# Kernel tuning notes

Hardware: AMD Instinct MI355X
Metric: run time of the kernel (lower is better)

Reference implementation:

```python
import jax, jax.numpy as jnp
import numpy as np

D_MODEL = 1024
N_HEADS = 16
D_K = D_MODEL // N_HEADS
B, L = 2, 2048


def setup_inputs() -> dict:
    key = jax.random.key(0)
    ks = jax.random.split(key, 13)
    s = 0.02
    inp = {
        'query': jax.random.normal(ks[0], (B, L, D_MODEL), jnp.float32),
        'key': jax.random.normal(ks[1], (B, L, D_MODEL), jnp.float32),
        'value': jax.random.normal(ks[2], (B, L, D_MODEL), jnp.float32),
        'mask': jax.random.randint(ks[3], (1, 1, L, L), 0, 2).astype(bool),
        'W_q': jax.random.normal(ks[4], (D_MODEL, D_MODEL), jnp.float32) * s,
        'b_q': jnp.zeros((D_MODEL,), jnp.float32),
        'W_k': jax.random.normal(ks[5], (D_MODEL, D_MODEL), jnp.float32) * s,
        'b_k': jnp.zeros((D_MODEL,), jnp.float32),
        'W_v': jax.random.normal(ks[6], (D_MODEL, D_MODEL), jnp.float32) * s,
        'b_v': jnp.zeros((D_MODEL,), jnp.float32),
        'W_o': jax.random.normal(ks[7], (D_MODEL, D_MODEL), jnp.float32) * s,
        'b_o': jnp.zeros((D_MODEL,), jnp.float32),
    }
    return inp


def _split_heads(x):
    b, l, _ = x.shape
    return x.reshape(b, l, N_HEADS, D_K).transpose(0, 2, 1, 3)  # [B,H,L,dk]


def reference(query, key, value, mask, W_q, b_q, W_k, b_k, W_v, b_v, W_o, b_o):
    q = _split_heads(query @ W_q + b_q)
    k = _split_heads(key @ W_k + b_k)
    v = _split_heads(value @ W_v + b_v)
    # Unscaled attention logits [B,H,L,L] (NO 1/sqrt(dk))
    logits = jnp.einsum('bhqd,bhkd->bhqk', q, k)
    logits = jnp.where(mask, -jnp.inf, logits)
    w = jax.nn.softmax(logits, axis=-1)
    w = jnp.nan_to_num(w, nan=0.0)  # fully-masked rows -> zeros
    attended = jnp.einsum('bhqk,bhkd->bhqd', w, v)
    # dropout in eval mode = identity; combine heads
    out = attended.transpose(0, 2, 1, 3).reshape(B, L, D_MODEL)
    return out @ W_o + b_o
```

## Files before the change

kernel.cpp:

```cpp
#include <hip/hip_runtime.h>
#include <hip/hip_bf16.h>
#include <stdint.h>


typedef __bf16 bf16;
typedef __bf16 bf16x8 __attribute__((ext_vector_type(8)));
typedef float f32x4 __attribute__((ext_vector_type(4)));

#define AS1 __attribute__((address_space(1)))
#define AS3 __attribute__((address_space(3)))

__device__ __forceinline__ void g2l16(const void* g, void* l) {
    __builtin_amdgcn_global_load_lds((AS1 void*)g, (AS3 void*)l, 16, 0, 0);
}

__device__ __forceinline__ bool lane_masked(unsigned long long m) {
#if __has_builtin(__builtin_amdgcn_inverse_ballot_w64)
    return __builtin_amdgcn_inverse_ballot_w64(m);
#else
    return (m >> (threadIdx.x & 63)) & 1ull;
#endif
}

#define LOG2E 1.44269504088896f

__global__ __launch_bounds__(256) void cvt3_kernel(const float* __restrict__ a0,
                                                   const float* __restrict__ a1,
                                                   const float* __restrict__ a2,
                                                   bf16* o0, bf16* o1, bf16* o2) {
    int y = blockIdx.y;
    const float* in = (y == 0) ? a0 : (y == 1) ? a1 : a2;
    bf16* out = (y == 0) ? o0 : (y == 1) ? o1 : o2;
    int idx = blockIdx.x * 256 + threadIdx.x;
    float4 v = ((const float4*)in)[idx];
    __align__(8) bf16 o[4];
    o[0] = (bf16)v.x; o[1] = (bf16)v.y; o[2] = (bf16)v.z; o[3] = (bf16)v.w;
    *(uint2*)(out + (size_t)idx * 4) = *(const uint2*)o;
}

__global__ __launch_bounds__(256) void mdetect_kernel(const unsigned int* __restrict__ w,
                                                      int* __restrict__ flag) {
    int idx = blockIdx.x * 256 + threadIdx.x;
    unsigned v = w[idx];
    int f = 0;
    if (v == 0x3F800000u) f = 2;
    else if (v > 1u) f = 1;
    unsigned long long b1 = __ballot(f & 1);
    unsigned long long b2 = __ballot(f & 2);
    if ((threadIdx.x & 63) == 0) {
        int agg = (b1 ? 1 : 0) | (b2 ? 2 : 0);
        if (agg) atomicOr(flag, agg);
    }
}

__global__ __launch_bounds__(256) void mpack_kernel(const void* __restrict__ mask,
                                                    unsigned long long* __restrict__ mb,
                                                    const int* __restrict__ flag) {
    int idx = blockIdx.x * 256 + threadIdx.x;
    int f = *flag;
    bool v;
    if (f & 2)      v = ((const float*)mask)[idx] != 0.0f;
    else if (f & 1) v = ((const unsigned char*)mask)[idx] != 0;
    else            v = ((const int*)mask)[idx] != 0;
    unsigned long long b = __ballot(v);
    if ((threadIdx.x & 63) == 0) mb[idx >> 6] = b;
}

__global__ __launch_bounds__(256) void rpack_kernel(const unsigned long long* __restrict__ mb,
                                                    unsigned long long* __restrict__ rmb) {
    int task = blockIdx.x * 4 + (threadIdx.x >> 6);
    int qg = task >> 5, kt = task & 31;
    int lane = threadIdx.x & 63, quad = lane >> 4, col = lane & 15;
    #pragma unroll
    for (int r = 0; r < 4; ++r) {
        unsigned long long wrow = mb[(size_t)(qg * 16 + quad * 4 + r) * 32 + kt];
        #pragma unroll
        for (int nt = 0; nt < 4; ++nt) {
            unsigned long long b = __ballot(((wrow >> (nt * 16 + col)) & 1ull) != 0);
            if (lane == 0) rmb[(size_t)task * 16 + r * 4 + nt] = b;
        }
    }
}

__global__ __launch_bounds__(256) void wtrans_kernel(const float* W0, const float* W1,
                                                     const float* W2, const float* W3,
                                                     bf16* T0, bf16* T1, bf16* T2, bf16* T3) {
    const float* W; bf16* T;
    int y = blockIdx.y;
    if (y == 0)      { W = W0; T = T0; }
    else if (y == 1) { W = W1; T = T1; }
    else if (y == 2) { W = W2; T = T2; }
    else             { W = W3; T = T3; }
    int tx = blockIdx.x & 15, ty = blockIdx.x >> 4;
    int n0 = tx * 64, k0 = ty * 64;
    __shared__ __align__(16) bf16 t[64 * 72];
    int tid = threadIdx.x;
    #pragma unroll
    for (int rr = 0; rr < 4; ++rr) {
        int idx = rr * 256 + tid;
        int r = idx >> 4, c4 = (idx & 15) * 4;
        float4 v = *(const float4*)(W + (size_t)(k0 + r) * 1024 + n0 + c4);
        __align__(8) bf16 o[4];
        o[0] = (bf16)v.x; o[1] = (bf16)v.y; o[2] = (bf16)v.z; o[3] = (bf16)v.w;
        *(uint2*)&t[r * 72 + c4] = *(const uint2*)o;
    }
    __syncthreads();
    #pragma unroll
    for (int rr = 0; rr < 2; ++rr) {
        int idx = rr * 256 + tid;
        int n = idx >> 3, kc = (idx & 7) * 8;
        __align__(16) bf16 o[8];
        #pragma unroll
        for (int j = 0; j < 8; ++j) o[j] = t[(kc + j) * 72 + n];
        *(uint4*)(T + (size_t)(n0 + n) * 1024 + k0 + kc) = *(const uint4*)o;
    }
}

template <int MODE>
__device__ __forceinline__ void gemm128_core(const bf16* __restrict__ A,
                                             const bf16* __restrict__ Bt,
                                             const float* __restrict__ bias,
                                             void* __restrict__ Out, int bm, int bn,
                                             float scale) {
    __shared__ __align__(16) bf16 la[128 * 32];
    __shared__ __align__(16) bf16 lb[128 * 32];
    int tid = threadIdx.x;
    int w = tid >> 6, lane = tid & 63;
    int quad = lane >> 4, col = lane & 15;
    int wm = w >> 1, wn = w & 1;
    int m0 = bm * 128, n0 = bn * 128;
    f32x4 acc[4][4];
    f32x4 z = {0.f, 0.f, 0.f, 0.f};
    #pragma unroll
    for (int i = 0; i < 4; ++i)
        #pragma unroll
        for (int j = 0; j < 4; ++j) acc[i][j] = z;
    int srow = lane >> 2;
    int skc = (lane & 3) * 8;
    for (int kt = 0; kt < 32; ++kt) {
        int kk = kt * 32;
        __syncthreads();
        #pragma unroll
        for (int rr = 0; rr < 2; ++rr) {
            int ch = rr * 4 + w;
            int row = ch * 16 + srow;
            g2l16(A + (size_t)(m0 + row) * 1024 + kk + skc, &la[ch * 512]);
            g2l16(Bt + (size_t)(n0 + row) * 1024 + kk + skc, &lb[ch * 512]);
        }
        __syncthreads();
        bf16x8 af[4], bfr[4];
        #pragma unroll
        for (int mt = 0; mt < 4; ++mt)
            af[mt] = *(const bf16x8*)&la[(wm * 64 + mt * 16 + col) * 32 + quad * 8];
        #pragma unroll
        for (int nt = 0; nt < 4; ++nt)
            bfr[nt] = *(const bf16x8*)&lb[(wn * 64 + nt * 16 + col) * 32 + quad * 8];
        #pragma unroll
        for (int mt = 0; mt < 4; ++mt)
            #pragma unroll
            for (int nt = 0; nt < 4; ++nt)
                acc[mt][nt] = __builtin_amdgcn_mfma_f32_16x16x32_bf16(
                    af[mt], bfr[nt], acc[mt][nt], 0, 0, 0);
    }
    float bia[4];
    #pragma unroll
    for (int nt = 0; nt < 4; ++nt) bia[nt] = bias[n0 + wn * 64 + nt * 16 + col];
    #pragma unroll
    for (int mt = 0; mt < 4; ++mt) {
        #pragma unroll
        for (int nt = 0; nt < 4; ++nt) {
            #pragma unroll
            for (int r = 0; r < 4; ++r) {
                int m = m0 + wm * 64 + mt * 16 + quad * 4 + r;
                int n = n0 + wn * 64 + nt * 16 + col;
                float v = (acc[mt][nt][r] + bia[nt]) * scale;
                if (MODE == 0) {
                    int b = m >> 11, l = m & 2047, h = n >> 6, d = n & 63;
                    ((bf16*)Out)[(((size_t)b * 16 + h) * 2048 + l) * 64 + d] = (bf16)v;
                } else {
                    int b = m >> 11, l = m & 2047, h = n >> 6, d = n & 63;
                    ((bf16*)Out)[(((size_t)b * 16 + h) * 64 + d) * 2048 + l] = (bf16)v;
                }
            }
        }
    }
}

__global__ __launch_bounds__(256) void qkv_kernel(
    const bf16* Xq, const bf16* Xk, const bf16* Xv,
    const bf16* Wq, const bf16* Wk, const bf16* Wv,
    const float* bq, const float* bk, const float* bv,
    bf16* Qh, bf16* Kh, bf16* Vt) {
    int y = blockIdx.y;
    int bm = blockIdx.x >> 3, bn = blockIdx.x & 7;
    if (y == 0)      gemm128_core<0>(Xq, Wq, bq, Qh, bm, bn, LOG2E);
    else if (y == 1) gemm128_core<0>(Xk, Wk, bk, Kh, bm, bn, 1.0f);
    else             gemm128_core<2>(Xv, Wv, bv, Vt, bm, bn, 1.0f);
}

__global__ __launch_bounds__(256) void ogemm_kernel(const bf16* __restrict__ A,
                                                    const bf16* __restrict__ Wt,
                                                    const float* __restrict__ bias,
                                                    float* __restrict__ Out) {
    int bm = blockIdx.x >> 3, bn = blockIdx.x & 7;
    __shared__ __align__(16) bf16 la[64 * 32];
    __shared__ __align__(16) bf16 lb[128 * 32];
    int tid = threadIdx.x;
    int w = tid >> 6, lane = tid & 63;
    int quad = lane >> 4, col = lane & 15;
    int m0 = bm * 64, n0 = bn * 128;
    f32x4 acc[4][2];
    f32x4 z = {0.f, 0.f, 0.f, 0.f};
    #pragma unroll
    for (int i = 0; i < 4; ++i) { acc[i][0] = z; acc[i][1] = z; }
    int srow = lane >> 2;
    int skc = (lane & 3) * 8;
    for (int kt = 0; kt < 32; ++kt) {
        int kk = kt * 32;
        __syncthreads();
        g2l16(A + (size_t)(m0 + w * 16 + srow) * 1024 + kk + skc, &la[w * 512]);
        #pragma unroll
        for (int rr = 0; rr < 2; ++rr) {
            int ch = rr * 4 + w;
            g2l16(Wt + (size_t)(n0 + ch * 16 + srow) * 1024 + kk + skc, &lb[ch * 512]);
        }
        __syncthreads();
        bf16x8 af[4], bfr[2];
        #pragma unroll
        for (int mt = 0; mt < 4; ++mt)
            af[mt] = *(const bf16x8*)&la[(mt * 16 + col) * 32 + quad * 8];
        #pragma unroll
        for (int nt = 0; nt < 2; ++nt)
            bfr[nt] = *(const bf16x8*)&lb[(w * 32 + nt * 16 + col) * 32 + quad * 8];
        #pragma unroll
        for (int mt = 0; mt < 4; ++mt)
            #pragma unroll
            for (int nt = 0; nt < 2; ++nt)
                acc[mt][nt] = __builtin_amdgcn_mfma_f32_16x16x32_bf16(
                    af[mt], bfr[nt], acc[mt][nt], 0, 0, 0);
    }
    float bia[2];
    bia[0] = bias[n0 + w * 32 + col];
    bia[1] = bias[n0 + w * 32 + 16 + col];
    #pragma unroll
    for (int mt = 0; mt < 4; ++mt)
        #pragma unroll
        for (int nt = 0; nt < 2; ++nt)
            #pragma unroll
            for (int r = 0; r < 4; ++r)
                Out[(size_t)(m0 + mt * 16 + quad * 4 + r) * 1024 +
                    n0 + w * 32 + nt * 16 + col] = acc[mt][nt][r] + bia[nt];
}

__global__ __launch_bounds__(128) void attn_kernel(const bf16* __restrict__ Qh,
                                                   const bf16* __restrict__ Kh,
                                                   const bf16* __restrict__ Vt,
                                                   const unsigned long long* __restrict__ rmb,
                                                   bf16* __restrict__ att) {
    int bh = blockIdx.x, qt = blockIdx.y;
    int b = bh >> 4, h = bh & 15;
    int q0 = qt * 64;
    __shared__ __align__(16) bf16 ks[64 * 64];
    __shared__ __align__(16) bf16 vs[64 * 64];
    __shared__ __align__(16) bf16 ps[2 * 32 * 72];
    int tid = threadIdx.x;
    int w = tid >> 6, lane = tid & 63;
    int quad = lane >> 4, col = lane & 15;
    int c7 = col & 7;
    int sr = lane >> 3;
    int sg = (lane & 7) ^ sr;
    int swz0 = (quad ^ c7) * 8;
    int swz1 = ((4 + quad) ^ c7) * 8;

    int mofs = __builtin_amdgcn_readfirstlane((qt * 4 + w * 2) * 512);

    #pragma unroll
    for (int i = 0; i < 4; ++i) {
        int ch = w * 4 + i;
        g2l16(Qh + ((size_t)bh * 2048 + q0 + ch * 8 + sr) * 64 + sg * 8, &ks[ch * 512]);
    }
    __syncthreads();
    bf16x8 aq[2][2];
    #pragma unroll
    for (int mt = 0; mt < 2; ++mt) {
        aq[mt][0] = *(const bf16x8*)&ks[(w * 32 + mt * 16 + col) * 64 + swz0];
        aq[mt][1] = *(const bf16x8*)&ks[(w * 32 + mt * 16 + col) * 64 + swz1];
    }
    bf16x8 onesf;
    #pragma unroll
    for (int i = 0; i < 8; ++i) onesf[i] = (bf16)1.0f;

    f32x4 z = {0.f, 0.f, 0.f, 0.f};
    f32x4 O[2][4], R[2];
    #pragma unroll
    for (int mt = 0; mt < 2; ++mt) {
        R[mt] = z;
        #pragma unroll
        for (int i = 0; i < 4; ++i) O[mt][i] = z;
    }

    for (int kt = 0; kt < 32; ++kt) {
        __syncthreads();
        #pragma unroll
        for (int i = 0; i < 4; ++i) {
            int ch = w * 4 + i;
            int r = ch * 8 + sr;
            g2l16(Kh + ((size_t)bh * 2048 + kt * 64 + r) * 64 + sg * 8, &ks[ch * 512]);
            g2l16(Vt + ((size_t)bh * 64 + r) * 2048 + kt * 64 + sg * 8, &vs[ch * 512]);
        }
        __syncthreads();

        f32x4 s[2][4];
        #pragma unroll
        for (int nt = 0; nt < 4; ++nt) {
            s[0][nt] = z; s[1][nt] = z;
            bf16x8 bk0 = *(const bf16x8*)&ks[(nt * 16 + col) * 64 + swz0];
            s[0][nt] = __builtin_amdgcn_mfma_f32_16x16x32_bf16(aq[0][0], bk0, s[0][nt], 0, 0, 0);
            s[1][nt] = __builtin_amdgcn_mfma_f32_16x16x32_bf16(aq[1][0], bk0, s[1][nt], 0, 0, 0);
            bf16x8 bk1 = *(const bf16x8*)&ks[(nt * 16 + col) * 64 + swz1];
            s[0][nt] = __builtin_amdgcn_mfma_f32_16x16x32_bf16(aq[0][1], bk1, s[0][nt], 0, 0, 0);
            s[1][nt] = __builtin_amdgcn_mfma_f32_16x16x32_bf16(aq[1][1], bk1, s[1][nt], 0, 0, 0);
        }

        #pragma unroll
        for (int mt = 0; mt < 2; ++mt) {
            const unsigned long long* mw = rmb + mofs + mt * 512 + kt * 16;
            #pragma unroll
            for (int r = 0; r < 4; ++r) {
                #pragma unroll
                for (int nt = 0; nt < 4; ++nt) {
                    float p = __builtin_amdgcn_exp2f(s[mt][nt][r]);
                    if (lane_masked(mw[r * 4 + nt])) p = 0.0f;
                    ps[w * 2304 + (mt * 16 + quad * 4 + r) * 72 + nt * 16 + col] = (bf16)p;
                }
            }
        }

        bf16x8 ap[2][2];
        #pragma unroll
        for (int mt = 0; mt < 2; ++mt) {
            ap[mt][0] = *(const bf16x8*)&ps[w * 2304 + (mt * 16 + col) * 72 + quad * 8];
            ap[mt][1] = *(const bf16x8*)&ps[w * 2304 + (mt * 16 + col) * 72 + 32 + quad * 8];
        }
        #pragma unroll
        for (int dt = 0; dt < 4; ++dt) {
            bf16x8 bv0 = *(const bf16x8*)&vs[(dt * 16 + col) * 64 + swz0];
            O[0][dt] = __builtin_amdgcn_mfma_f32_16x16x32_bf16(ap[0][0], bv0, O[0][dt], 0, 0, 0);
            O[1][dt] = __builtin_amdgcn_mfma_f32_16x16x32_bf16(ap[1][0], bv0, O[1][dt], 0, 0, 0);
            bf16x8 bv1 = *(const bf16x8*)&vs[(dt * 16 + col) * 64 + swz1];
            O[0][dt] = __builtin_amdgcn_mfma_f32_16x16x32_bf16(ap[0][1], bv1, O[0][dt], 0, 0, 0);
            O[1][dt] = __builtin_amdgcn_mfma_f32_16x16x32_bf16(ap[1][1], bv1, O[1][dt], 0, 0, 0);
        }
        #pragma unroll
        for (int mt = 0; mt < 2; ++mt) {
            R[mt] = __builtin_amdgcn_mfma_f32_16x16x32_bf16(ap[mt][0], onesf, R[mt], 0, 0, 0);
            R[mt] = __builtin_amdgcn_mfma_f32_16x16x32_bf16(ap[mt][1], onesf, R[mt], 0, 0, 0);
        }
    }

    #pragma unroll
    for (int mt = 0; mt < 2; ++mt) {
        #pragma unroll
        for (int r = 0; r < 4; ++r) {
            float rsv = R[mt][r];
            float inv = (rsv > 0.f) ? 1.0f / rsv : 0.f;
            int qg = q0 + w * 32 + mt * 16 + quad * 4 + r;
            #pragma unroll
            for (int dt = 0; dt < 4; ++dt) {
                float ov = O[mt][dt][r] * inv;
                att[((size_t)b * 2048 + qg) * 1024 + h * 64 + dt * 16 + col] = (bf16)ov;
            }
        }
    }
}

extern "C" void kernel_launch(void* const* d_in, const int* in_sizes, int n_in,
                              void* d_out, int out_size, void* d_ws, size_t ws_size,
                              hipStream_t stream) {
    (void)in_sizes; (void)n_in; (void)out_size; (void)ws_size;
    const float* query = (const float*)d_in[0];
    const float* key_  = (const float*)d_in[1];
    const float* value = (const float*)d_in[2];
    const void*  mask  = d_in[3];
    const float* W_q = (const float*)d_in[4];
    const float* b_q = (const float*)d_in[5];
    const float* W_k = (const float*)d_in[6];
    const float* b_k = (const float*)d_in[7];
    const float* W_v = (const float*)d_in[8];
    const float* b_v = (const float*)d_in[9];
    const float* W_o = (const float*)d_in[10];
    const float* b_o = (const float*)d_in[11];

    char* ws = (char*)d_ws;
    bf16* Xq  = (bf16*)(ws + 0);
    bf16* Xk  = (bf16*)(ws + 8388608);
    bf16* Xv  = (bf16*)(ws + 16777216);
    bf16* Wtq = (bf16*)(ws + 25165824);
    bf16* Wtk = (bf16*)(ws + 27262976);
    bf16* Wtv = (bf16*)(ws + 29360128);
    bf16* Wto = (bf16*)(ws + 31457280);
    bf16* Qh  = (bf16*)(ws + 33554432);
    bf16* Kh  = (bf16*)(ws + 41943040);
    bf16* Vt  = (bf16*)(ws + 50331648);
    bf16* att = (bf16*)(ws + 58720256);
    unsigned long long* mb  = (unsigned long long*)(ws + 67108864);
    unsigned long long* rmb = (unsigned long long*)(ws + 67633152);
    int* flag = (int*)(ws + 68157440);

    hipMemsetAsync(flag, 0, 4, stream);
    mdetect_kernel<<<4096, 256, 0, stream>>>((const unsigned int*)mask, flag);
    mpack_kernel<<<16384, 256, 0, stream>>>(mask, mb, flag);
    rpack_kernel<<<1024, 256, 0, stream>>>(mb, rmb);

    cvt3_kernel<<<dim3(4096, 3), 256, 0, stream>>>(query, key_, value, Xq, Xk, Xv);
    wtrans_kernel<<<dim3(256, 4), 256, 0, stream>>>(W_q, W_k, W_v, W_o, Wtq, Wtk, Wtv, Wto);

    qkv_kernel<<<dim3(256, 3), 256, 0, stream>>>(Xq, Xk, Xv, Wtq, Wtk, Wtv,
                                                 b_q, b_k, b_v, Qh, Kh, Vt);
    attn_kernel<<<dim3(32, 32), 128, 0, stream>>>(Qh, Kh, Vt, rmb, att);
    ogemm_kernel<<<512, 256, 0, stream>>>(att, Wto, b_o, (float*)d_out);
}
```

Before: 271.8 us.

## Fuse input conversion into GEMMs, split attention over keys, merge mask packing

Measured after the change: 297.4 us. +9.4%, slower.

```diff
diff --git a/kernel.cpp b/kernel.cpp
--- a/kernel.cpp
+++ b/kernel.cpp
@@ -23,20 +23,6 @@
 }
 
 #define LOG2E 1.44269504088896f
-
-__global__ __launch_bounds__(256) void cvt3_kernel(const float* __restrict__ a0,
-                                                   const float* __restrict__ a1,
-                                                   const float* __restrict__ a2,
-                                                   bf16* o0, bf16* o1, bf16* o2) {
-    int y = blockIdx.y;
-    const float* in = (y == 0) ? a0 : (y == 1) ? a1 : a2;
-    bf16* out = (y == 0) ? o0 : (y == 1) ? o1 : o2;
-    int idx = blockIdx.x * 256 + threadIdx.x;
-    float4 v = ((const float4*)in)[idx];
-    __align__(8) bf16 o[4];
-    o[0] = (bf16)v.x; o[1] = (bf16)v.y; o[2] = (bf16)v.z; o[3] = (bf16)v.w;
-    *(uint2*)(out + (size_t)idx * 4) = *(const uint2*)o;
-}
 
 __global__ __launch_bounds__(256) void mdetect_kernel(const unsigned int* __restrict__ w,
                                                       int* __restrict__ flag) {
@@ -53,30 +39,24 @@
     }
 }
 
-__global__ __launch_bounds__(256) void mpack_kernel(const void* __restrict__ mask,
-                                                    unsigned long long* __restrict__ mb,
-                                                    const int* __restrict__ flag) {
-    int idx = blockIdx.x * 256 + threadIdx.x;
-    int f = *flag;
-    bool v;
-    if (f & 2)      v = ((const float*)mask)[idx] != 0.0f;
-    else if (f & 1) v = ((const unsigned char*)mask)[idx] != 0;
-    else            v = ((const int*)mask)[idx] != 0;
-    unsigned long long b = __ballot(v);
-    if ((threadIdx.x & 63) == 0) mb[idx >> 6] = b;
-}
-
-__global__ __launch_bounds__(256) void rpack_kernel(const unsigned long long* __restrict__ mb,
-                                                    unsigned long long* __restrict__ rmb) {
+__global__ __launch_bounds__(256) void rpack2_kernel(const void* __restrict__ mask,
+                                                     const int* __restrict__ flag,
+                                                     unsigned long long* __restrict__ rmb) {
     int task = blockIdx.x * 4 + (threadIdx.x >> 6);
     int qg = task >> 5, kt = task & 31;
     int lane = threadIdx.x & 63, quad = lane >> 4, col = lane & 15;
+    int f = *flag;
     #pragma unroll
     for (int r = 0; r < 4; ++r) {
-        unsigned long long wrow = mb[(size_t)(qg * 16 + quad * 4 + r) * 32 + kt];
+        int row = qg * 16 + quad * 4 + r;
         #pragma unroll
         for (int nt = 0; nt < 4; ++nt) {
-            unsigned long long b = __ballot(((wrow >> (nt * 16 + col)) & 1ull) != 0);
+            size_t e = (size_t)row * 2048 + kt * 64 + nt * 16 + col;
+            bool v;
+            if (f & 2)      v = ((const float*)mask)[e] != 0.0f;
+            else if (f & 1) v = ((const unsigned char*)mask)[e] != 0;
+            else            v = ((const int*)mask)[e] != 0;
+            unsigned long long b = __ballot(v);
             if (lane == 0) rmb[(size_t)task * 16 + r * 4 + nt] = b;
         }
     }
@@ -117,7 +97,7 @@
 }
 
 template <int MODE>
-__device__ __forceinline__ void gemm128_core(const bf16* __restrict__ A,
+__device__ __forceinline__ void gemm128_core(const float* __restrict__ A,
                                              const bf16* __restrict__ Bt,
                                              const float* __restrict__ bias,
                                              void* __restrict__ Out, int bm, int bn,
@@ -144,7 +124,13 @@
         for (int rr = 0; rr < 2; ++rr) {
             int ch = rr * 4 + w;
             int row = ch * 16 + srow;
-            g2l16(A + (size_t)(m0 + row) * 1024 + kk + skc, &la[ch * 512]);
+            const float* ap_ = A + (size_t)(m0 + row) * 1024 + kk + skc;
+            float4 v0 = *(const float4*)ap_;
+            float4 v1 = *(const float4*)(ap_ + 4);
+            __align__(16) bf16 o[8];
+            o[0] = (bf16)v0.x; o[1] = (bf16)v0.y; o[2] = (bf16)v0.z; o[3] = (bf16)v0.w;
+            o[4] = (bf16)v1.x; o[5] = (bf16)v1.y; o[6] = (bf16)v1.z; o[7] = (bf16)v1.w;
+            *(uint4*)&la[ch * 512 + lane * 8] = *(const uint4*)o;
             g2l16(Bt + (size_t)(n0 + row) * 1024 + kk + skc, &lb[ch * 512]);
         }
         __syncthreads();
@@ -187,7 +173,7 @@
 }
 
 __global__ __launch_bounds__(256) void qkv_kernel(
-    const bf16* Xq, const bf16* Xk, const bf16* Xv,
+    const float* Xq, const float* Xk, const float* Xv,
     const bf16* Wq, const bf16* Wk, const bf16* Wv,
     const float* bq, const float* bk, const float* bv,
     bf16* Qh, bf16* Kh, bf16* Vt) {
@@ -198,7 +184,106 @@
     else             gemm128_core<2>(Xv, Wv, bv, Vt, bm, bn, 1.0f);
 }
 
-__global__ __launch_bounds__(256) void ogemm_kernel(const bf16* __restrict__ A,
+__global__ __launch_bounds__(256, 6) void attn_kernel(const bf16* __restrict__ Qh,
+                                                      const bf16* __restrict__ Kh,
+                                                      const bf16* __restrict__ Vt,
+                                                      const unsigned long long* __restrict__ rmb,
+                                                      float* __restrict__ Op,
+                                                      float* __restrict__ Rp) {
+    int bh = blockIdx.x, qt = blockIdx.y, zz = blockIdx.z;
+    int q0 = qt * 64;
+    __shared__ __align__(16) bf16 ks[64 * 64];
+    __shared__ __align__(16) bf16 vs[64 * 64];
+    __shared__ __align__(16) bf16 ps[4 * 16 * 72];
+    int tid = threadIdx.x;
+    int w = tid >> 6, lane = tid & 63;
+    int quad = lane >> 4, col = lane & 15;
+    int c7 = col & 7;
+    int sr = lane >> 3;
+    int sg = (lane & 7) ^ sr;
+    int swz0 = (quad ^ c7) * 8;
+    int swz1 = ((4 + quad) ^ c7) * 8;
+
+    int mofs = __builtin_amdgcn_readfirstlane((qt * 4 + w) * 512);
+
+    #pragma unroll
+    for (int i = 0; i < 2; ++i) {
+        int ch = w * 2 + i;
+        g2l16(Qh + ((size_t)bh * 2048 + q0 + ch * 8 + sr) * 64 + sg * 8, &ks[ch * 512]);
+    }
+    __syncthreads();
+    bf16x8 aq[2];
+    aq[0] = *(const bf16x8*)&ks[(w * 16 + col) * 64 + swz0];
+    aq[1] = *(const bf16x8*)&ks[(w * 16 + col) * 64 + swz1];
+    bf16x8 onesf;
+    #pragma unroll
+    for (int i = 0; i < 8; ++i) onesf[i] = (bf16)1.0f;
+
+    f32x4 z = {0.f, 0.f, 0.f, 0.f};
+    f32x4 O[4], R1 = z;
+    #pragma unroll
+    for (int i = 0; i < 4; ++i) O[i] = z;
+
+    for (int it = 0; it < 16; ++it) {
+        int kt = zz * 16 + it;
+        __syncthreads();
+        #pragma unroll
+        for (int i = 0; i < 2; ++i) {
+            int ch = w * 2 + i;
+            int r = ch * 8 + sr;
+            g2l16(Kh + ((size_t)bh * 2048 + kt * 64 + r) * 64 + sg * 8, &ks[ch * 512]);
+            g2l16(Vt + ((size_t)bh * 64 + r) * 2048 + kt * 64 + sg * 8, &vs[ch * 512]);
+        }
+        __syncthreads();
+
+        f32x4 s[4];
+        #pragma unroll
+        for (int nt = 0; nt < 4; ++nt) {
+            s[nt] = z;
+            bf16x8 bk0 = *(const bf16x8*)&ks[(nt * 16 + col) * 64 + swz0];
+            s[nt] = __builtin_amdgcn_mfma_f32_16x16x32_bf16(aq[0], bk0, s[nt], 0, 0, 0);
+            bf16x8 bk1 = *(const bf16x8*)&ks[(nt * 16 + col) * 64 + swz1];
+            s[nt] = __builtin_amdgcn_mfma_f32_16x16x32_bf16(aq[1], bk1, s[nt], 0, 0, 0);
+        }
+
+        const unsigned long long* mw = rmb + mofs + kt * 16;
+        #pragma unroll
+        for (int r = 0; r < 4; ++r) {
+            #pragma unroll
+            for (int nt = 0; nt < 4; ++nt) {
+                float p = __builtin_amdgcn_exp2f(s[nt][r]);
+                if (lane_masked(mw[r * 4 + nt])) p = 0.0f;
+                ps[w * 1152 + (quad * 4 + r) * 72 + nt * 16 + col] = (bf16)p;
+            }
+        }
+
+        bf16x8 ap0 = *(const bf16x8*)&ps[w * 1152 + col * 72 + quad * 8];
+        bf16x8 ap1 = *(const bf16x8*)&ps[w * 1152 + col * 72 + 32 + quad * 8];
+        #pragma unroll
+        for (int dt = 0; dt < 4; ++dt) {
+            bf16x8 bv0 = *(const bf16x8*)&vs[(dt * 16 + col) * 64 + swz0];
+            O[dt] = __builtin_amdgcn_mfma_f32_16x16x32_bf16(ap0, bv0, O[dt], 0, 0, 0);
+            bf16x8 bv1 = *(const bf16x8*)&vs[(dt * 16 + col) * 64 + swz1];
+            O[dt] = __builtin_amdgcn_mfma_f32_16x16x32_bf16(ap1, bv1, O[dt], 0, 0, 0);
+        }
+        R1 = __builtin_amdgcn_mfma_f32_16x16x32_bf16(ap0, onesf, R1, 0, 0, 0);
+        R1 = __builtin_amdgcn_mfma_f32_16x16x32_bf16(ap1, onesf, R1, 0, 0, 0);
+    }
+
+    size_t pb = (size_t)(zz * 1024 + bh * 32 + qt);
+    size_t obase = pb * 4096;
+    #pragma unroll
+    for (int r = 0; r < 4; ++r) {
+        int q = w * 16 + quad * 4 + r;
+        #pragma unroll
+        for (int dt = 0; dt < 4; ++dt)
+            Op[obase + (size_t)q * 64 + dt * 16 + col] = O[dt][r];
+        if (col == 0) Rp[pb * 64 + q] = R1[r];
+    }
+}
+
+__global__ __launch_bounds__(256) void ogemm_kernel(const float* __restrict__ Op,
+                                                    const float* __restrict__ Rp,
                                                     const bf16* __restrict__ Wt,
                                                     const float* __restrict__ bias,
                                                     float* __restrict__ Out) {
@@ -215,10 +300,31 @@
     for (int i = 0; i < 4; ++i) { acc[i][0] = z; acc[i][1] = z; }
     int srow = lane >> 2;
     int skc = (lane & 3) * 8;
+    int m = m0 + w * 16 + srow;
+    int b = m >> 11, l = m & 2047;
+    int qt = l >> 6, q = l & 63;
     for (int kt = 0; kt < 32; ++kt) {
         int kk = kt * 32;
         __syncthreads();
-        g2l16(A + (size_t)(m0 + w * 16 + srow) * 1024 + kk + skc, &la[w * 512]);
+        {
+            int kc = kk + skc;
+            int h = kc >> 6, d0 = kc & 63;
+            int bhq = (b * 16 + h) * 32 + qt;
+            size_t base = (size_t)bhq * 4096 + (size_t)q * 64 + d0;
+            f32x4 a00 = *(const f32x4*)(Op + base);
+            f32x4 a01 = *(const f32x4*)(Op + base + 4);
+            f32x4 a10 = *(const f32x4*)(Op + 4194304 + base);
+            f32x4 a11 = *(const f32x4*)(Op + 4194304 + base + 4);
+            float rsum = Rp[(size_t)bhq * 64 + q] + Rp[65536 + (size_t)bhq * 64 + q];
+            float inv = (rsum > 0.f) ? __builtin_amdgcn_rcpf(rsum) : 0.f;
+            __align__(16) bf16 o[8];
+            #pragma unroll
+            for (int i = 0; i < 4; ++i) {
+                o[i]     = (bf16)((a00[i] + a10[i]) * inv);
+                o[i + 4] = (bf16)((a01[i] + a11[i]) * inv);
+            }
+            *(uint4*)&la[w * 512 + lane * 8] = *(const uint4*)o;
+        }
         #pragma unroll
         for (int rr = 0; rr < 2; ++rr) {
             int ch = rr * 4 + w;
@@ -250,128 +356,6 @@
             for (int r = 0; r < 4; ++r)
                 Out[(size_t)(m0 + mt * 16 + quad * 4 + r) * 1024 +
                     n0 + w * 32 + nt * 16 + col] = acc[mt][nt][r] + bia[nt];
-}
-
-__global__ __launch_bounds__(128) void attn_kernel(const bf16* __restrict__ Qh,
-                                                   const bf16* __restrict__ Kh,
-                                                   const bf16* __restrict__ Vt,
-                                                   const unsigned long long* __restrict__ rmb,
-                                                   bf16* __restrict__ att) {
-    int bh = blockIdx.x, qt = blockIdx.y;
-    int b = bh >> 4, h = bh & 15;
-    int q0 = qt * 64;
-    __shared__ __align__(16) bf16 ks[64 * 64];
-    __shared__ __align__(16) bf16 vs[64 * 64];
-    __shared__ __align__(16) bf16 ps[2 * 32 * 72];
-    int tid = threadIdx.x;
-    int w = tid >> 6, lane = tid & 63;
-    int quad = lane >> 4, col = lane & 15;
-    int c7 = col & 7;
-    int sr = lane >> 3;
-    int sg = (lane & 7) ^ sr;
-    int swz0 = (quad ^ c7) * 8;
-    int swz1 = ((4 + quad) ^ c7) * 8;
-
-    int mofs = __builtin_amdgcn_readfirstlane((qt * 4 + w * 2) * 512);
-
-    #pragma unroll
-    for (int i = 0; i < 4; ++i) {
-        int ch = w * 4 + i;
-        g2l16(Qh + ((size_t)bh * 2048 + q0 + ch * 8 + sr) * 64 + sg * 8, &ks[ch * 512]);
-    }
-    __syncthreads();
-    bf16x8 aq[2][2];
-    #pragma unroll
-    for (int mt = 0; mt < 2; ++mt) {
-        aq[mt][0] = *(const bf16x8*)&ks[(w * 32 + mt * 16 + col) * 64 + swz0];
-        aq[mt][1] = *(const bf16x8*)&ks[(w * 32 + mt * 16 + col) * 64 + swz1];
-    }
-    bf16x8 onesf;
-    #pragma unroll
-    for (int i = 0; i < 8; ++i) onesf[i] = (bf16)1.0f;
-
-    f32x4 z = {0.f, 0.f, 0.f, 0.f};
-    f32x4 O[2][4], R[2];
-    #pragma unroll
-    for (int mt = 0; mt < 2; ++mt) {
-        R[mt] = z;
-        #pragma unroll
-        for (int i = 0; i < 4; ++i) O[mt][i] = z;
-    }
-
-    for (int kt = 0; kt < 32; ++kt) {
-        __syncthreads();
-        #pragma unroll
-        for (int i = 0; i < 4; ++i) {
-            int ch = w * 4 + i;
-            int r = ch * 8 + sr;
-            g2l16(Kh + ((size_t)bh * 2048 + kt * 64 + r) * 64 + sg * 8, &ks[ch * 512]);
-            g2l16(Vt + ((size_t)bh * 64 + r) * 2048 + kt * 64 + sg * 8, &vs[ch * 512]);
-        }
-        __syncthreads();
-
-        f32x4 s[2][4];
-        #pragma unroll
-        for (int nt = 0; nt < 4; ++nt) {
-            s[0][nt] = z; s[1][nt] = z;
-            bf16x8 bk0 = *(const bf16x8*)&ks[(nt * 16 + col) * 64 + swz0];
-            s[0][nt] = __builtin_amdgcn_mfma_f32_16x16x32_bf16(aq[0][0], bk0, s[0][nt], 0, 0, 0);
-            s[1][nt] = __builtin_amdgcn_mfma_f32_16x16x32_bf16(aq[1][0], bk0, s[1][nt], 0, 0, 0);
-            bf16x8 bk1 = *(const bf16x8*)&ks[(nt * 16 + col) * 64 + swz1];
-            s[0][nt] = __builtin_amdgcn_mfma_f32_16x16x32_bf16(aq[0][1], bk1, s[0][nt], 0, 0, 0);
-            s[1][nt] = __builtin_amdgcn_mfma_f32_16x16x32_bf16(aq[1][1], bk1, s[1][nt], 0, 0, 0);
-        }
-
-        #pragma unroll
-        for (int mt = 0; mt < 2; ++mt) {
-            const unsigned long long* mw = rmb + mofs + mt * 512 + kt * 16;
-            #pragma unroll
-            for (int r = 0; r < 4; ++r) {
-                #pragma unroll
-                for (int nt = 0; nt < 4; ++nt) {
-                    float p = __builtin_amdgcn_exp2f(s[mt][nt][r]);
-                    if (lane_masked(mw[r * 4 + nt])) p = 0.0f;
-                    ps[w * 2304 + (mt * 16 + quad * 4 + r) * 72 + nt * 16 + col] = (bf16)p;
-                }
-            }
-        }
-
-        bf16x8 ap[2][2];
-        #pragma unroll
-        for (int mt = 0; mt < 2; ++mt) {
-            ap[mt][0] = *(const bf16x8*)&ps[w * 2304 + (mt * 16 + col) * 72 + quad * 8];
-            ap[mt][1] = *(const bf16x8*)&ps[w * 2304 + (mt * 16 + col) * 72 + 32 + quad * 8];
-        }
-        #pragma unroll
-        for (int dt = 0; dt < 4; ++dt) {
-            bf16x8 bv0 = *(const bf16x8*)&vs[(dt * 16 + col) * 64 + swz0];
-            O[0][dt] = __builtin_amdgcn_mfma_f32_16x16x32_bf16(ap[0][0], bv0, O[0][dt], 0, 0, 0);
-            O[1][dt] = __builtin_amdgcn_mfma_f32_16x16x32_bf16(ap[1][0], bv0, O[1][dt], 0, 0, 0);
-            bf16x8 bv1 = *(const bf16x8*)&vs[(dt * 16 + col) * 64 + swz1];
-            O[0][dt] = __builtin_amdgcn_mfma_f32_16x16x32_bf16(ap[0][1], bv1, O[0][dt], 0, 0, 0);
-            O[1][dt] = __builtin_amdgcn_mfma_f32_16x16x32_bf16(ap[1][1], bv1, O[1][dt], 0, 0, 0);
-        }
-        #pragma unroll
-        for (int mt = 0; mt < 2; ++mt) {
-            R[mt] = __builtin_amdgcn_mfma_f32_16x16x32_bf16(ap[mt][0], onesf, R[mt], 0, 0, 0);
-            R[mt] = __builtin_amdgcn_mfma_f32_16x16x32_bf16(ap[mt][1], onesf, R[mt], 0, 0, 0);
-        }
-    }
-
-    #pragma unroll
-    for (int mt = 0; mt < 2; ++mt) {
-        #pragma unroll
-        for (int r = 0; r < 4; ++r) {
-            float rsv = R[mt][r];
-            float inv = (rsv > 0.f) ? 1.0f / rsv : 0.f;
-            int qg = q0 + w * 32 + mt * 16 + quad * 4 + r;
-            #pragma unroll
-            for (int dt = 0; dt < 4; ++dt) {
-                float ov = O[mt][dt][r] * inv;
-                att[((size_t)b * 2048 + qg) * 1024 + h * 64 + dt * 16 + col] = (bf16)ov;
-            }
-        }
-    }
 }
 
 extern "C" void kernel_launch(void* const* d_in, const int* in_sizes, int n_in,
@@ -392,31 +376,25 @@
     const float* b_o = (const float*)d_in[11];
 
     char* ws = (char*)d_ws;
-    bf16* Xq  = (bf16*)(ws + 0);
-    bf16* Xk  = (bf16*)(ws + 8388608);
-    bf16* Xv  = (bf16*)(ws + 16777216);
+    bf16* Qh  = (bf16*)(ws + 0);
+    bf16* Kh  = (bf16*)(ws + 8388608);
+    bf16* Vt  = (bf16*)(ws + 16777216);
     bf16* Wtq = (bf16*)(ws + 25165824);
     bf16* Wtk = (bf16*)(ws + 27262976);
     bf16* Wtv = (bf16*)(ws + 29360128);
     bf16* Wto = (bf16*)(ws + 31457280);
-    bf16* Qh  = (bf16*)(ws + 33554432);
-    bf16* Kh  = (bf16*)(ws + 41943040);
-    bf16* Vt  = (bf16*)(ws + 50331648);
-    bf16* att = (bf16*)(ws + 58720256);
-    unsigned long long* mb  = (unsigned long long*)(ws + 67108864);
+    float* Op = (float*)(ws + 33554432);
+    float* Rp = (float*)(ws + 67108864);
     unsigned long long* rmb = (unsigned long long*)(ws + 67633152);
     int* flag = (int*)(ws + 68157440);
 
     hipMemsetAsync(flag, 0, 4, stream);
     mdetect_kernel<<<4096, 256, 0, stream>>>((const unsigned int*)mask, flag);
-    mpack_kernel<<<16384, 256, 0, stream>>>(mask, mb, flag);
-    rpack_kernel<<<1024, 256, 0, stream>>>(mb, rmb);
-
-    cvt3_kernel<<<dim3(4096, 3), 256, 0, stream>>>(query, key_, value, Xq, Xk, Xv);
+    rpack2_kernel<<<1024, 256, 0, stream>>>(mask, flag, rmb);
+
     wtrans_kernel<<<dim3(256, 4), 256, 0, stream>>>(W_q, W_k, W_v, W_o, Wtq, Wtk, Wtv, Wto);
-
-    qkv_kernel<<<dim3(256, 3), 256, 0, stream>>>(Xq, Xk, Xv, Wtq, Wtk, Wtv,
+    qkv_kernel<<<dim3(256, 3), 256, 0, stream>>>(query, key_, value, Wtq, Wtk, Wtv,
                                                  b_q, b_k, b_v, Qh, Kh, Vt);
-    attn_kernel<<<dim3(32, 32), 128, 0, stream>>>(Qh, Kh, Vt, rmb, att);
-    ogemm_kernel<<<512, 256, 0, stream>>>(att, Wto, b_o, (float*)d_out);
-}
+    attn_kernel<<<dim3(32, 32, 2), 256, 0, stream>>>(Qh, Kh, Vt, rmb, Op, Rp);
+    ogemm_kernel<<<512, 256, 0, stream>>>(Op, Rp, Wto, b_o, (float*)d_out);
+}
```
